# Kernel tuning notes

Hardware: AMD Instinct MI355X
Metric: run time of the kernel (lower is better)

## Reference

```python
import jax, jax.numpy as jnp
import numpy as np

BS, QLEN, KLEN = 2, 64, 64
N_HEADS, D_KV = 8, 64
INNER = N_HEADS * D_KV  # 512
VOCAB = 4096


def _layernorm(x, g, b, eps=1e-6):
    m = jnp.mean(x, axis=-1, keepdims=True)
    v = jnp.mean(jnp.square(x - m), axis=-1, keepdims=True)
    return (x - m) * jax.lax.rsqrt(v + eps) * g + b


def _l2norm(x, eps=1e-12):
    sq = jnp.sum(jnp.square(x), axis=-1, keepdims=True)
    return x * jax.lax.rsqrt(jnp.maximum(sq, eps))


def setup_inputs() -> dict:
    key = jax.random.key(0)
    ks = jax.random.split(key, 8)
    d = {
        'query': jax.random.normal(ks[0], (BS, QLEN, INNER), jnp.float32),
        'key': jax.random.normal(ks[1], (BS, KLEN, INNER), jnp.float32),
        'q_position_embeddings': jax.random.normal(ks[2], (BS, QLEN, INNER), jnp.float32),
        'k_position_embeddings': jax.random.normal(ks[3], (BS, KLEN, INNER), jnp.float32),
        'wi_w': jax.random.normal(ks[4], (2 * INNER, INNER), jnp.float32) / np.sqrt(2 * INNER),
        'vq_dict': jax.random.normal(ks[5], (VOCAB, D_KV), jnp.float32) * np.sqrt(2.0 / (VOCAB + D_KV)),
        'vq_ln_g': jnp.ones((D_KV,), jnp.float32),
        'vq_ln_b': jnp.zeros((D_KV,), jnp.float32),
        'vq_o_w': jax.random.normal(ks[6], (D_KV, D_KV), jnp.float32) / np.sqrt(D_KV),
        'ln_g': jnp.ones((D_KV,), jnp.float32),
        'ln_b': jnp.zeros((D_KV,), jnp.float32),
    }
    return d


def reference(query, key, q_position_embeddings, k_position_embeddings,
              wi_w, vq_dict, vq_ln_g, vq_ln_b, vq_o_w, ln_g, ln_b):
    bs, qlen, dim = query.shape
    klen = key.shape[1]

    q = query + q_position_embeddings
    k = key + k_position_embeddings
    # wi(concat([q, 0])) == q @ wi_w[:dim]; wi(concat([0, k])) == k @ wi_w[dim:]
    q_proj = jnp.einsum('bqd,de->bqe', q, wi_w[:dim])   # [bs, qlen, inner]
    k_proj = jnp.einsum('bkd,de->bke', k, wi_w[dim:])   # [bs, klen, inner]

    # pairwise outer sum -> [bs, qlen, klen, inner] -> tokens of size d_kv
    rcr = q_proj[:, :, None, :] + k_proj[:, None, :, :]
    y = rcr.reshape(bs, qlen * klen * N_HEADS, D_KV)

    # --- VectorQuantizer (eval mode: no dropout, loss = 0) ---
    y_n = _l2norm(y)
    d_n = _l2norm(vq_dict)
    sim = jnp.einsum('bnd,vd->bnv', y_n, d_n)           # [bs, N, vocab]
    word_idx = jnp.argmax(sim, axis=-1)                 # [bs, N] int
    word_sim = jnp.max(sim, axis=-1)                    # [bs, N]
    z = vq_dict[word_idx]                               # gather
    emb = jax.lax.stop_gradient(z - y) + y              # straight-through
    emb = _layernorm(emb, vq_ln_g, vq_ln_b)
    emb = jnp.einsum('bnd,de->bne', emb, vq_o_w)

    r3 = emb.reshape(bs, qlen, klen, N_HEADS, D_KV)
    r3_scores = word_sim.reshape(bs, qlen, klen, N_HEADS, 1)
    out_ids = word_idx.reshape(bs, qlen, klen, N_HEADS, 1)

    r3_weighted = jnp.mean(r3 * r3_scores, axis=2)      # [bs, qlen, n_heads, d_kv]
    r3_weighted = jnp.transpose(r3_weighted, (0, 2, 1, 3))  # [bs, n_heads, qlen, d_kv]
    r3_weighted = _layernorm(r3_weighted, ln_g, ln_b)
    return r3_weighted, out_ids, r3_scores
```

## Files before the change

kernel.cpp:

```cpp
#include <hip/hip_runtime.h>
#include <math.h>

#define BS 2
#define QLEN 64
#define KLEN 64
#define NH 8
#define DKV 64
#define INNER 512
#define VOCAB 4096
#define CHUNKV 64
#define RS 129
#define BUFD (CHUNKV * RS)

typedef double vdbl4 __attribute__((ext_vector_type(4)));


__global__ __launch_bounds__(256) void k_prep(
    const float* __restrict__ q_in, const float* __restrict__ k_in,
    const float* __restrict__ qpe, const float* __restrict__ kpe,
    const float* __restrict__ wi,
    const float* __restrict__ vq, const float* __restrict__ g,
    const float* __restrict__ bta, const float* __restrict__ ow,
    double* __restrict__ qp, double* __restrict__ kp,
    double* __restrict__ dnt, float* __restrict__ E,
    unsigned long long* __restrict__ bestf)
{
    __shared__ double S[3200];
    int bid = blockIdx.x;
    int t = threadIdx.x;

    if (bid < 512) {
        int side = bid >> 8;
        int b    = (bid >> 7) & 1;
        int rp   = (bid >> 2) & 31;
        int cq   = bid & 3;
        const float* xin = side ? k_in : q_in;
        const float* pin = side ? kpe : qpe;
        double* outp = side ? kp : qp;
        int wrow0 = side ? INNER : 0;
        int r0 = rp * 2;
        double* xs = S;
        double* red = S + 1024;
        for (int i = t; i < 2 * INNER; i += 256) {
            int rr = i >> 9, dd = i & 511;
            int gidx = (b * 64 + r0 + rr) * INNER + dd;
            xs[rr * INNER + dd] = (double)xin[gidx] + (double)pin[gidx];
        }
        __syncthreads();
        int col = cq * 128 + (t & 127);
        int dh = t >> 7;
        double a0 = 0.0, a1 = 0.0;
        #pragma unroll 8
        for (int d = dh * 256; d < dh * 256 + 256; ++d) {
            double w = (double)wi[(size_t)(wrow0 + d) * INNER + col];
            a0 = fma(xs[d], w, a0);
            a1 = fma(xs[INNER + d], w, a1);
        }
        red[t] = a0;
        red[256 + t] = a1;
        __syncthreads();
        if (t < 128) {
            outp[(size_t)(b * 64 + r0) * INNER + cq * 128 + t] = red[t] + red[t + 128];
            outp[(size_t)(b * 64 + r0 + 1) * INNER + cq * 128 + t] = red[256 + t] + red[256 + t + 128];
        }
    } else {
        int db = bid - 512;
        bestf[db * 256 + t] = 0ull;
        double* Dsh = S;
        float*  Osh = (float*)(S + 1088);
        int vb = db * 16;
        int wv = t >> 6, lane = t & 63;
        for (int i = t; i < 4096; i += 256) Osh[i] = ow[i];
        __syncthreads();
        for (int ii = 0; ii < 4; ++ii) {
            int vloc = wv * 4 + ii;
            int v = vb + vloc;
            double z = (double)vq[v * DKV + lane];
            double s2 = z * z, s1 = z;
            for (int m = 32; m >= 1; m >>= 1) { s2 += __shfl_xor(s2, m); s1 += __shfl_xor(s1, m); }
            Dsh[lane * 17 + vloc] = z * (1.0 / sqrt(fmax(s2, 1e-12)));
            double mean = s1 * (1.0 / 64.0);
            double d0 = z - mean;
            double vv2 = d0 * d0;
            for (int m = 32; m >= 1; m >>= 1) vv2 += __shfl_xor(vv2, m);
            vv2 *= (1.0 / 64.0);
            double ln = d0 * (1.0 / sqrt(vv2 + 1e-6)) * (double)g[lane] + (double)bta[lane];
            double acc = 0.0;
            for (int jj = 0; jj < 64; ++jj)
                acc = fma(__shfl(ln, jj), (double)Osh[jj * 64 + lane], acc);
            E[v * DKV + lane] = (float)acc;
        }
        __syncthreads();
        for (int i = t; i < 1024; i += 256) {
            int j = i >> 4, vloc = i & 15;
            dnt[(size_t)j * VOCAB + vb + vloc] = Dsh[j * 17 + vloc];
        }
    }
}

__global__ __launch_bounds__(1024, 4) void k_simscan(
    const double* __restrict__ qp, const double* __restrict__ kp,
    const double* __restrict__ dnt,
    unsigned long long* __restrict__ bestf)
{
    int bid = blockIdx.x;
    int bh = bid & 15, cg = bid >> 4;
    int b = bh >> 3, h = bh & 7;
    int t = threadIdx.x;
    int w = t >> 6, l = t & 63;

    __shared__ double S[2 * BUFD];

    int asub = l >> 4;
    int lrow = l & 15;
    bool isprod = (w < 8);

    int drow[4], dcol[4];
    {
        vdbl4 prow = (vdbl4){0.0, 0.0, 0.0, 0.0};
        vdbl4 pcol = (vdbl4){0.0, 0.0, 0.0, 0.0};
        double a_row = (asub == 0) ? (double)lrow : 0.0;
        double b_one = (asub == 0) ? 1.0 : 0.0;
        double a_one = (asub == 0) ? 1.0 : 0.0;
        double b_col = (asub == 0) ? (double)lrow : 0.0;
        prow = __builtin_amdgcn_mfma_f64_16x16x4f64(a_row, b_one, prow, 0, 0, 0);
        pcol = __builtin_amdgcn_mfma_f64_16x16x4f64(a_one, b_col, pcol, 0, 0, 0);
        #pragma unroll
        for (int r = 0; r < 4; ++r) { drow[r] = (int)prow[r]; dcol[r] = (int)pcol[r]; }
    }

    double afr[16];
    if (isprod) {
        const double* src = (w < 4) ? qp : kp;
        int arow = (w & 3) * 16 + lrow;
        #pragma unroll
        for (int ks = 0; ks < 16; ++ks)
            afr[ks] = src[(size_t)(b * 64 + arow) * INNER + h * 64 + ks * 4 + asub];
    }

    int ci = t - 512;
    int qg = ci & 15, kg = (ci >> 4) & 31;
    double best[4][2];
    #pragma unroll
    for (int i = 0; i < 4; ++i)
        #pragma unroll
        for (int j = 0; j < 2; ++j) best[i][j] = 0.0;

    for (int step = 0; step < 5; ++step) {
        if (isprod && step < 4) {
            int v0 = (cg * 4 + step) * CHUNKV;
            double* buf = S + (step & 1) * BUFD;
            vdbl4 acc[4];
            #pragma unroll
            for (int vt = 0; vt < 4; ++vt) acc[vt] = (vdbl4){0.0, 0.0, 0.0, 0.0};
            size_t base = (size_t)asub * VOCAB + v0 + lrow;
            double bcur[4], bnext[4];
            #pragma unroll
            for (int vt = 0; vt < 4; ++vt) bcur[vt] = dnt[base + vt * 16];
            #pragma unroll
            for (int ks = 0; ks < 16; ++ks) {
                if (ks < 15) {
                    size_t krow = base + (size_t)((ks + 1) * 4) * VOCAB;
                    #pragma unroll
                    for (int vt = 0; vt < 4; ++vt) bnext[vt] = dnt[krow + vt * 16];
                }
                #pragma unroll
                for (int vt = 0; vt < 4; ++vt)
                    acc[vt] = __builtin_amdgcn_mfma_f64_16x16x4f64(
                        afr[ks], bcur[vt], acc[vt], 0, 0, 0);
                if (ks < 15) {
                    #pragma unroll
                    for (int vt = 0; vt < 4; ++vt) bcur[vt] = bnext[vt];
                }
            }
            bool isq = (w < 4);
            int rbase = (isq ? 0 : 64) + (w & 3) * 16;
            #pragma unroll
            for (int vt = 0; vt < 4; ++vt)
                #pragma unroll
                for (int r = 0; r < 4; ++r) {
                    int vl = vt * 16 + dcol[r];
                    unsigned long long code =
                        (unsigned long long)((4095 - (v0 + vl)) << 1);
                    double s = fma(acc[vt][r], 1.0 / 64.0, 1.5);
                    unsigned long long bb2 = __double_as_longlong(s) & ~0x1FFFull;
                    if (isq) bb2 |= code;
                    buf[vl * RS + rbase + drow[r]] = __longlong_as_double(bb2);
                }
        }
        if (!isprod && step >= 1) {
            double* buf = S + ((step - 1) & 1) * BUFD;
            #pragma unroll 2
            for (int v = 0; v < CHUNKV; ++v) {
                double qv[4], kv[2];
                #pragma unroll
                for (int i = 0; i < 4; ++i) qv[i] = buf[v * RS + qg + 16 * i];
                #pragma unroll
                for (int j = 0; j < 2; ++j) kv[j] = buf[v * RS + 64 + kg + 32 * j];
                #pragma unroll
                for (int i = 0; i < 4; ++i)
                    #pragma unroll
                    for (int j = 0; j < 2; ++j)
                        best[i][j] = fmax(best[i][j], qv[i] + kv[j]);
            }
        }
        if (step < 4) __syncthreads();
    }

    if (!isprod) {
        #pragma unroll
        for (int i = 0; i < 4; ++i)
            #pragma unroll
            for (int j = 0; j < 2; ++j) {
                int q = qg + 16 * i, k = kg + 32 * j;
                atomicMax(&bestf[((size_t)bh * 64 + q) * 64 + k],
                          (unsigned long long)__double_as_longlong(best[i][j]));
            }
    }
}

__global__ __launch_bounds__(256) void k_combine(
    const unsigned long long* __restrict__ bestf,
    const double* __restrict__ qp, const double* __restrict__ kp,
    const float* __restrict__ E,
    const float* __restrict__ lng, const float* __restrict__ lnb,
    float* __restrict__ out)
{
    int bid = blockIdx.x;
    int bh = bid >> 4, qg = bid & 15;
    int b = bh >> 3, h = bh & 7;
    int t = threadIdx.x;
    int w = t >> 6, lane = t & 63;
    int q0 = qg * 4;

    __shared__ double SC[4416];
    double* qs_l = SC;
    double* ks_l = SC + 256;
    __shared__ float ws_l[4][64];
    __shared__ int  idx_l[4][64];

    {
        int row = t >> 6, d = t & 63;
        qs_l[row * 64 + d] = qp[(size_t)(b * 64 + q0 + row) * INNER + h * 64 + d];
    }
    for (int i = t; i < 4096; i += 256) {
        int kr = i >> 6, d = i & 63;
        ks_l[kr * 65 + d] = kp[(size_t)(b * 64 + kr) * INNER + h * 64 + d];
    }
    __syncthreads();

    int qq = t >> 6;
    int k = t & 63;
    int q = q0 + qq;
    double gdot = 0.0, qn2 = 0.0, kn2 = 0.0;
    for (int d = 0; d < 64; ++d) {
        double xq = qs_l[qq * 64 + d];
        double xk = ks_l[k * 65 + d];
        gdot = fma(xq, xk, gdot);
        qn2 = fma(xq, xq, qn2);
        kn2 = fma(xk, xk, kn2);
    }

    unsigned long long bb = bestf[((size_t)bh * 64 + q) * 64 + k];
    int vidx = 4095 - (int)(bb & 0xFFFull);
    double sval = __longlong_as_double(bb & ~0x1FFFull);
    double tru = (sval - 3.0) * 64.0;
    double n2 = qn2 + kn2 + 2.0 * gdot;
    double wsim = tru * (1.0 / sqrt(fmax(n2, 1e-12)));

    size_t oidx = ((size_t)(b * QLEN + q) * KLEN + k) * NH + h;
    out[65536 + oidx] = (float)vidx;
    out[131072 + oidx] = (float)wsim;

    ws_l[w][k] = (float)wsim;
    idx_l[w][k] = vidx;
    __syncthreads();

    int d = lane;
    float acc = 0.0f;
    for (int k2 = 0; k2 < 64; ++k2)
        acc += E[idx_l[w][k2] * DKV + d] * ws_l[w][k2];
    acc *= (1.0f / 64.0f);
    float mean = acc;
    for (int m = 32; m >= 1; m >>= 1) mean += __shfl_xor(mean, m);
    mean *= (1.0f / 64.0f);
    float dv = acc - mean;
    float var = dv * dv;
    for (int m = 32; m >= 1; m >>= 1) var += __shfl_xor(var, m);
    var *= (1.0f / 64.0f);
    float o = dv * rsqrtf(var + 1e-6f) * lng[d] + lnb[d];
    out[(((size_t)b * NH + h) * QLEN + q) * DKV + d] = o;
}

extern "C" void kernel_launch(void* const* d_in, const int* in_sizes, int n_in,
                              void* d_out, int out_size, void* d_ws, size_t ws_size,
                              hipStream_t stream) {
    const float* query = (const float*)d_in[0];
    const float* key   = (const float*)d_in[1];
    const float* qpe   = (const float*)d_in[2];
    const float* kpe   = (const float*)d_in[3];
    const float* wi    = (const float*)d_in[4];
    const float* vq    = (const float*)d_in[5];
    const float* vqg   = (const float*)d_in[6];
    const float* vqb   = (const float*)d_in[7];
    const float* ow    = (const float*)d_in[8];
    const float* lng   = (const float*)d_in[9];
    const float* lnb   = (const float*)d_in[10];
    float* out = (float*)d_out;

    char* ws = (char*)d_ws;
    double* qp  = (double*)(ws + 0);
    double* kp  = (double*)(ws + 524288);
    double* dnt = (double*)(ws + 1048576);
    float*  E   = (float*) (ws + 3145728);
    unsigned long long* bestf = (unsigned long long*)(ws + 4194304);

    k_prep   <<<768, 256, 0, stream>>>(query, key, qpe, kpe, wi, vq, vqg, vqb, ow,
                                       qp, kp, dnt, E, bestf);
    k_simscan<<<256, 1024, 0, stream>>>(qp, kp, dnt, bestf);
    k_combine<<<256, 256, 0, stream>>>(bestf, qp, kp, E, lng, lnb, out);
}
```

Measured before the change: 172.5 us.

## Permute simscan LDS layout for vector loads and split prep into more blocks

The shared-memory buffer in the similarity scan is re-laid out so each thread's four q values and two k values sit next to each other (row stride 130), which lets the max-plus inner loop use 128-bit vector LDS loads instead of six scalar loads. The prep kernel is split across more, finer blocks: projection columns go from 128 to 64 per block, and dictionary normalisation handles one vocab row per wave with a shared-memory matvec instead of shuffles. The goal is fewer LDS instructions in the hot scan and more parallelism in prep. The permuted writes may add bank conflicts on the producer side.

```diff
diff --git a/kernel.cpp b/kernel.cpp
--- a/kernel.cpp
+++ b/kernel.cpp
@@ -9,10 +9,11 @@
 #define INNER 512
 #define VOCAB 4096
 #define CHUNKV 64
-#define RS 129
+#define RS 130
 #define BUFD (CHUNKV * RS)
 
 typedef double vdbl4 __attribute__((ext_vector_type(4)));
+typedef double vdbl2 __attribute__((ext_vector_type(2)));
 
 
 __global__ __launch_bounds__(256) void k_prep(
@@ -25,15 +26,16 @@
     double* __restrict__ dnt, float* __restrict__ E,
     unsigned long long* __restrict__ bestf)
 {
-    __shared__ double S[3200];
+    __shared__ double S[1600];
+    __shared__ float Osh[4096];
     int bid = blockIdx.x;
     int t = threadIdx.x;
 
-    if (bid < 512) {
-        int side = bid >> 8;
-        int b    = (bid >> 7) & 1;
-        int rp   = (bid >> 2) & 31;
-        int cq   = bid & 3;
+    if (bid < 1024) {
+        int side = bid >> 9;
+        int b    = (bid >> 8) & 1;
+        int rp   = (bid >> 3) & 31;
+        int cb   = bid & 7;
         const float* xin = side ? k_in : q_in;
         const float* pin = side ? kpe : qpe;
         double* outp = side ? kp : qp;
@@ -47,53 +49,57 @@
             xs[rr * INNER + dd] = (double)xin[gidx] + (double)pin[gidx];
         }
         __syncthreads();
-        int col = cq * 128 + (t & 127);
-        int dh = t >> 7;
+        int col = cb * 64 + (t & 63);
+        int dh = t >> 6;
         double a0 = 0.0, a1 = 0.0;
         #pragma unroll 8
-        for (int d = dh * 256; d < dh * 256 + 256; ++d) {
+        for (int d = dh * 128; d < dh * 128 + 128; ++d) {
             double w = (double)wi[(size_t)(wrow0 + d) * INNER + col];
             a0 = fma(xs[d], w, a0);
             a1 = fma(xs[INNER + d], w, a1);
         }
-        red[t] = a0;
-        red[256 + t] = a1;
+        red[(dh * 2 + 0) * 64 + (t & 63)] = a0;
+        red[(dh * 2 + 1) * 64 + (t & 63)] = a1;
         __syncthreads();
         if (t < 128) {
-            outp[(size_t)(b * 64 + r0) * INNER + cq * 128 + t] = red[t] + red[t + 128];
-            outp[(size_t)(b * 64 + r0 + 1) * INNER + cq * 128 + t] = red[256 + t] + red[256 + t + 128];
+            int rr = t >> 6, c2 = t & 63;
+            double s = (red[(0 * 2 + rr) * 64 + c2] + red[(1 * 2 + rr) * 64 + c2])
+                     + (red[(2 * 2 + rr) * 64 + c2] + red[(3 * 2 + rr) * 64 + c2]);
+            outp[(size_t)(b * 64 + r0 + rr) * INNER + cb * 64 + c2] = s;
         }
     } else {
-        int db = bid - 512;
-        bestf[db * 256 + t] = 0ull;
-        double* Dsh = S;
-        float*  Osh = (float*)(S + 1088);
-        int vb = db * 16;
+        int db = bid - 1024;
+        if (db < 256) bestf[db * 256 + t] = 0ull;
+        double* Lsh = S;
+        double* Dsh = S + 256;
+        int vb = db * 4;
         int wv = t >> 6, lane = t & 63;
         for (int i = t; i < 4096; i += 256) Osh[i] = ow[i];
+        int v = vb + wv;
+        double z = (double)vq[v * DKV + lane];
+        double s2 = z * z, s1 = z;
+        for (int m = 32; m >= 1; m >>= 1) { s2 += __shfl_xor(s2, m); s1 += __shfl_xor(s1, m); }
+        Dsh[lane * 5 + wv] = z * (1.0 / sqrt(fmax(s2, 1e-12)));
+        double mean = s1 * (1.0 / 64.0);
+        double d0 = z - mean;
+        double vv2 = d0 * d0;
+        for (int m = 32; m >= 1; m >>= 1) vv2 += __shfl_xor(vv2, m);
+        vv2 *= (1.0 / 64.0);
+        Lsh[wv * 64 + lane] = d0 * (1.0 / sqrt(vv2 + 1e-6)) * (double)g[lane] + (double)bta[lane];
         __syncthreads();
-        for (int ii = 0; ii < 4; ++ii) {
-            int vloc = wv * 4 + ii;
-            int v = vb + vloc;
-            double z = (double)vq[v * DKV + lane];
-            double s2 = z * z, s1 = z;
-            for (int m = 32; m >= 1; m >>= 1) { s2 += __shfl_xor(s2, m); s1 += __shfl_xor(s1, m); }
-            Dsh[lane * 17 + vloc] = z * (1.0 / sqrt(fmax(s2, 1e-12)));
-            double mean = s1 * (1.0 / 64.0);
-            double d0 = z - mean;
-            double vv2 = d0 * d0;
-            for (int m = 32; m >= 1; m >>= 1) vv2 += __shfl_xor(vv2, m);
-            vv2 *= (1.0 / 64.0);
-            double ln = d0 * (1.0 / sqrt(vv2 + 1e-6)) * (double)g[lane] + (double)bta[lane];
-            double acc = 0.0;
-            for (int jj = 0; jj < 64; ++jj)
-                acc = fma(__shfl(ln, jj), (double)Osh[jj * 64 + lane], acc);
-            E[v * DKV + lane] = (float)acc;
-        }
-        __syncthreads();
-        for (int i = t; i < 1024; i += 256) {
-            int j = i >> 4, vloc = i & 15;
-            dnt[(size_t)j * VOCAB + vb + vloc] = Dsh[j * 17 + vloc];
+        double c0 = 0.0, c1 = 0.0, c2 = 0.0, c3 = 0.0;
+        #pragma unroll 4
+        for (int gg = 0; gg < 16; ++gg) {
+            int jj = gg * 4;
+            c0 = fma(Lsh[wv * 64 + jj + 0], (double)Osh[(jj + 0) * 64 + lane], c0);
+            c1 = fma(Lsh[wv * 64 + jj + 1], (double)Osh[(jj + 1) * 64 + lane], c1);
+            c2 = fma(Lsh[wv * 64 + jj + 2], (double)Osh[(jj + 2) * 64 + lane], c2);
+            c3 = fma(Lsh[wv * 64 + jj + 3], (double)Osh[(jj + 3) * 64 + lane], c3);
+        }
+        E[v * DKV + lane] = (float)((c0 + c1) + (c2 + c3));
+        {
+            int j = t >> 2, vloc = t & 3;
+            dnt[(size_t)j * VOCAB + vb + vloc] = Dsh[j * 5 + vloc];
         }
     }
 }
@@ -174,34 +180,37 @@
                 }
             }
             bool isq = (w < 4);
-            int rbase = (isq ? 0 : 64) + (w & 3) * 16;
             #pragma unroll
             for (int vt = 0; vt < 4; ++vt)
                 #pragma unroll
                 for (int r = 0; r < 4; ++r) {
                     int vl = vt * 16 + dcol[r];
+                    int grow = (w & 3) * 16 + drow[r];
+                    int slot = isq ? ((grow & 15) * 4 + (grow >> 4))
+                                   : (64 + (grow & 31) * 2 + (grow >> 5));
                     unsigned long long code =
                         (unsigned long long)((4095 - (v0 + vl)) << 1);
                     double s = fma(acc[vt][r], 1.0 / 64.0, 1.5);
                     unsigned long long bb2 = __double_as_longlong(s) & ~0x1FFFull;
                     if (isq) bb2 |= code;
-                    buf[vl * RS + rbase + drow[r]] = __longlong_as_double(bb2);
+                    buf[vl * RS + slot] = __longlong_as_double(bb2);
                 }
         }
         if (!isprod && step >= 1) {
             double* buf = S + ((step - 1) & 1) * BUFD;
             #pragma unroll 2
             for (int v = 0; v < CHUNKV; ++v) {
-                double qv[4], kv[2];
-                #pragma unroll
-                for (int i = 0; i < 4; ++i) qv[i] = buf[v * RS + qg + 16 * i];
-                #pragma unroll
-                for (int j = 0; j < 2; ++j) kv[j] = buf[v * RS + 64 + kg + 32 * j];
-                #pragma unroll
-                for (int i = 0; i < 4; ++i)
-                    #pragma unroll
-                    for (int j = 0; j < 2; ++j)
-                        best[i][j] = fmax(best[i][j], qv[i] + kv[j]);
+                vdbl2 q01 = *(const vdbl2*)&buf[v * RS + qg * 4];
+                vdbl2 q23 = *(const vdbl2*)&buf[v * RS + qg * 4 + 2];
+                vdbl2 k01 = *(const vdbl2*)&buf[v * RS + 64 + kg * 2];
+                best[0][0] = fmax(best[0][0], q01[0] + k01[0]);
+                best[0][1] = fmax(best[0][1], q01[0] + k01[1]);
+                best[1][0] = fmax(best[1][0], q01[1] + k01[0]);
+                best[1][1] = fmax(best[1][1], q01[1] + k01[1]);
+                best[2][0] = fmax(best[2][0], q23[0] + k01[0]);
+                best[2][1] = fmax(best[2][1], q23[0] + k01[1]);
+                best[3][0] = fmax(best[3][0], q23[1] + k01[0]);
+                best[3][1] = fmax(best[3][1], q23[1] + k01[1]);
             }
         }
         if (step < 4) __syncthreads();
@@ -315,8 +324,8 @@
     float*  E   = (float*) (ws + 3145728);
     unsigned long long* bestf = (unsigned long long*)(ws + 4194304);
 
-    k_prep   <<<768, 256, 0, stream>>>(query, key, qpe, kpe, wi, vq, vqg, vqb, ow,
-                                       qp, kp, dnt, E, bestf);
+    k_prep   <<<2048, 256, 0, stream>>>(query, key, qpe, kpe, wi, vq, vqg, vqb, ow,
+                                        qp, kp, dnt, E, bestf);
     k_simscan<<<256, 1024, 0, stream>>>(qp, kp, dnt, bestf);
     k_combine<<<256, 256, 0, stream>>>(bestf, qp, kp, E, lng, lnb, out);
 }
```

Result: faster. 154.9 us (-10.2%).
